# Kernel optimization log

Hardware: AMD Instinct MI355X
Metric: run time of the kernel (lower is better)

Reference implementation:

```python
import jax, jax.numpy as jnp
import numpy as np

T, B, IN, H, OUT = 345, 128, 13, 128, 9

# snnTorch ATan surrogate spike: forward = heaviside(x), backward = 1/(1+(pi*x)^2) (alpha=2)
@jax.custom_vjp
def spike_fn(x):
    return (x > 0).astype(x.dtype)

def _spike_fwd(x):
    return spike_fn(x), x

def _spike_bwd(x, g):
    return (g / (1.0 + (jnp.pi * x) ** 2),)

spike_fn.defvjp(_spike_fwd, _spike_bwd)


def setup_inputs() -> dict:
    key = jax.random.key(0)
    ks = jax.random.split(key, 5)
    x = jax.random.normal(ks[0], (B, IN, T), dtype=jnp.float32)
    # PyTorch Linear init: U(-1/sqrt(fan_in), 1/sqrt(fan_in))
    lim1 = 1.0 / np.sqrt(IN)
    lim2 = 1.0 / np.sqrt(H)
    W1 = jax.random.uniform(ks[1], (H, IN), minval=-lim1, maxval=lim1, dtype=jnp.float32)
    b1 = jax.random.uniform(ks[2], (H,), minval=-lim1, maxval=lim1, dtype=jnp.float32)
    W2 = jax.random.uniform(ks[3], (OUT, H), minval=-lim2, maxval=lim2, dtype=jnp.float32)
    b2 = jax.random.uniform(ks[4], (OUT,), minval=-lim2, maxval=lim2, dtype=jnp.float32)
    beta1 = jnp.float32(0.9)
    thr1 = jnp.float32(1.0)
    beta2 = jnp.float32(0.9)
    thr2 = jnp.float32(1.0)
    return {"x": x, "W1": W1, "b1": b1, "W2": W2, "b2": b2,
            "beta1": beta1, "thr1": thr1, "beta2": beta2, "thr2": thr2}


def reference(x, W1, b1, W2, b2, beta1, thr1, beta2, thr2):
    # Precompute fc1 for all steps: (T, B, H)
    cur1_all = jnp.einsum('bct,hc->tbh', x, W1) + b1
    bt1 = jnp.clip(beta1, 0.0, 1.0)
    bt2 = jnp.clip(beta2, 0.0, 1.0)

    def step(carry, cur1):
        mem1, mem2 = carry
        mem1 = bt1 * mem1 + cur1                 # leaky integrate
        spk1 = spike_fn(mem1 - thr1)             # fire
        mem1 = mem1 - spk1 * thr1                # subtract reset
        cur2 = spk1 @ W2.T + b2                  # (B, OUT)
        mem2 = bt2 * mem2 + cur2
        spk2 = spike_fn(mem2 - thr2)
        mem2 = mem2 - spk2 * thr2
        return (mem1, mem2), (spk2, mem2)

    init = (jnp.zeros((B, H), x.dtype), jnp.zeros((B, OUT), x.dtype))
    _, (spk_rec, mem_rec) = jax.lax.scan(step, init, cur1_all)
    return spk_rec, mem_rec  # each (T, B, OUT)
```

## Files before the change

### kernel.cpp

```cpp
#include <hip/hip_runtime.h>

#define T_STEPS 345
#define B_SZ    128
#define IN_SZ   13
#define H_SZ    128
#define OUT_SZ  9
#define XPITCH  16
#define TPAD    384
#define NBO     (B_SZ * OUT_SZ)
#define NCHUNK  22
#define MASK_BYTES (B_SZ * T_STEPS * 2 * 8)

__global__ __launch_bounds__(128, 1)
void k1_spikes(const float* __restrict__ x, const float* __restrict__ W1,
               const float* __restrict__ b1, const float* __restrict__ beta1p,
               const float* __restrict__ thr1p,
               unsigned long long* __restrict__ masks)
{
    const int b   = blockIdx.x;
    const int tid = threadIdx.x;

    __shared__ float xst[(T_STEPS + 3) * XPITCH];

    const float* xb = x + (size_t)b * (IN_SZ * T_STEPS);
    for (int i = tid; i < IN_SZ * T_STEPS; i += 128) {
        const int c = i / T_STEPS;
        const int t = i - c * T_STEPS;
        xst[t * XPITCH + c] = xb[i];
    }

    const float bt1 = fminf(fmaxf(beta1p[0], 0.0f), 1.0f);
    const float th1 = thr1p[0];

    float w1r[IN_SZ];
#pragma unroll
    for (int c = 0; c < IN_SZ; ++c) w1r[c] = W1[tid * IN_SZ + c];
    const float b1r = b1[tid];

    float mem1 = 0.0f;
    unsigned long long* mp = masks + (size_t)b * (T_STEPS * 2) + (tid >> 6);
    const bool store_lane = (tid & 63) == 0;

    __syncthreads();

    const float4* xq = (const float4*)xst;
    float4 a0 = xq[0], a1 = xq[1], a2 = xq[2]; float a3 = xst[12];
    float4 c0 = xq[4], c1 = xq[5], c2 = xq[6]; float c3 = xst[XPITCH + 12];

    int t = 0;
    for (; t < T_STEPS - 1; t += 2) {
        const float xa[IN_SZ] = { a0.x,a0.y,a0.z,a0.w, a1.x,a1.y,a1.z,a1.w,
                                  a2.x,a2.y,a2.z,a2.w, a3 };
        const float xc[IN_SZ] = { c0.x,c0.y,c0.z,c0.w, c1.x,c1.y,c1.z,c1.w,
                                  c2.x,c2.y,c2.z,c2.w, c3 };
        a0 = xq[(t+2)*4+0]; a1 = xq[(t+2)*4+1]; a2 = xq[(t+2)*4+2]; a3 = xst[(t+2)*XPITCH+12];
        c0 = xq[(t+3)*4+0]; c1 = xq[(t+3)*4+1]; c2 = xq[(t+3)*4+2]; c3 = xst[(t+3)*XPITCH+12];

        float cura = b1r, curb = b1r;
#pragma unroll
        for (int c = 0; c < IN_SZ; ++c) {
            cura = fmaf(xa[c], w1r[c], cura);
            curb = fmaf(xc[c], w1r[c], curb);
        }

        mem1 = fmaf(bt1, mem1, cura);
        const bool pa = mem1 > th1;
        const unsigned long long ma = __ballot(pa);
        mem1 = fmaf(pa ? -1.0f : 0.0f, th1, mem1);
        if (store_lane) mp[0] = ma;

        mem1 = fmaf(bt1, mem1, curb);
        const bool pb = mem1 > th1;
        const unsigned long long mb = __ballot(pb);
        mem1 = fmaf(pb ? -1.0f : 0.0f, th1, mem1);
        if (store_lane) mp[2] = mb;

        mp += 4;
    }
    {
        const float xa[IN_SZ] = { a0.x,a0.y,a0.z,a0.w, a1.x,a1.y,a1.z,a1.w,
                                  a2.x,a2.y,a2.z,a2.w, a3 };
        float cura = b1r;
#pragma unroll
        for (int c = 0; c < IN_SZ; ++c) cura = fmaf(xa[c], w1r[c], cura);
        mem1 = fmaf(bt1, mem1, cura);
        const bool pa = mem1 > th1;
        const unsigned long long ma = __ballot(pa);
        if (store_lane) mp[0] = ma;
    }
}

__global__ __launch_bounds__(256, 1)
void k2_gemm(const unsigned long long* __restrict__ masks,
             const float* __restrict__ W2, const float* __restrict__ b2,
             float* __restrict__ cur2)
{
    const int gw   = blockIdx.x * 4 + (threadIdx.x >> 6);
    const int lane = threadIdx.x & 63;
    const int bo   = gw / 6;
    const int w    = gw - bo * 6;
    const int b    = bo / 9;
    const int o    = bo - b * 9;
    const int t    = w * 64 + lane;
    const int tc   = (t < T_STEPS) ? t : (T_STEPS - 1);

    const uint4 mm = *(const uint4*)((const char*)masks +
                                     ((size_t)b * T_STEPS + tc) * 16);

    const float* __restrict__ w2row = W2 + o * H_SZ;
    float acc = 0.0f;
#pragma unroll
    for (int h = 0; h < 32; ++h)
        acc = fmaf((float)((mm.x >> h) & 1u), w2row[h], acc);
#pragma unroll
    for (int h = 0; h < 32; ++h)
        acc = fmaf((float)((mm.y >> h) & 1u), w2row[32 + h], acc);
#pragma unroll
    for (int h = 0; h < 32; ++h)
        acc = fmaf((float)((mm.z >> h) & 1u), w2row[64 + h], acc);
#pragma unroll
    for (int h = 0; h < 32; ++h)
        acc = fmaf((float)((mm.w >> h) & 1u), w2row[96 + h], acc);

    cur2[(size_t)t * NBO + bo] = acc + b2[o];
}

__global__ __launch_bounds__(64, 1)
void k3_scan2(const float* __restrict__ cur2, const float* __restrict__ beta2p,
              const float* __restrict__ thr2p, float* __restrict__ out)
{
    const int lid = blockIdx.x * 64 + threadIdx.x;
    const float bt2 = fminf(fmaxf(beta2p[0], 0.0f), 1.0f);
    const float th2 = thr2p[0];

    const float* __restrict__ src = cur2 + lid;
    float* __restrict__ out_spk = out + lid;
    float* __restrict__ out_mem = out + (size_t)T_STEPS * NBO + lid;

    float mem2 = 0.0f;

    float A[16], Bb[16];
#pragma unroll
    for (int j = 0; j < 16; ++j) A[j]  = src[(size_t)j * NBO];
#pragma unroll
    for (int j = 0; j < 16; ++j) Bb[j] = src[(size_t)(16 + j) * NBO];

    float sE[16], mE[16], sO[16], mO[16];

    for (int c = 0; c < NCHUNK; c += 2) {
#pragma unroll
        for (int j = 0; j < 16; ++j) {
            mem2 = fmaf(bt2, mem2, A[j]);
            const float sp = (mem2 > th2) ? 1.0f : 0.0f;
            mem2 = fmaf(-sp, th2, mem2);
            sE[j] = sp; mE[j] = mem2;
        }
        const int cn = (c + 2 < NCHUNK) ? (c + 2) : c;
#pragma unroll
        for (int j = 0; j < 16; ++j) A[j] = src[(size_t)(cn * 16 + j) * NBO];
        {
            const size_t base = (size_t)c * 16 * NBO;
#pragma unroll
            for (int j = 0; j < 16; ++j) {
                out_spk[base + (size_t)j * NBO] = sE[j];
                out_mem[base + (size_t)j * NBO] = mE[j];
            }
        }

#pragma unroll
        for (int j = 0; j < 16; ++j) {
            mem2 = fmaf(bt2, mem2, Bb[j]);
            const float sp = (mem2 > th2) ? 1.0f : 0.0f;
            mem2 = fmaf(-sp, th2, mem2);
            sO[j] = sp; mO[j] = mem2;
        }
        const int cn2 = (c + 3 < NCHUNK) ? (c + 3) : c;
#pragma unroll
        for (int j = 0; j < 16; ++j) Bb[j] = src[(size_t)(cn2 * 16 + j) * NBO];
        if (c + 1 < NCHUNK - 1) {
            const size_t base = (size_t)(c + 1) * 16 * NBO;
#pragma unroll
            for (int j = 0; j < 16; ++j) {
                out_spk[base + (size_t)j * NBO] = sO[j];
                out_mem[base + (size_t)j * NBO] = mO[j];
            }
        } else {
            const size_t base = (size_t)(c + 1) * 16 * NBO;
#pragma unroll
            for (int j = 0; j < 9; ++j) {
                out_spk[base + (size_t)j * NBO] = sO[j];
                out_mem[base + (size_t)j * NBO] = mO[j];
            }
        }
    }
}

extern "C" void kernel_launch(void* const* d_in, const int* in_sizes, int n_in,
                              void* d_out, int out_size, void* d_ws, size_t ws_size,
                              hipStream_t stream) {
    const float* x     = (const float*)d_in[0];
    const float* W1    = (const float*)d_in[1];
    const float* b1    = (const float*)d_in[2];
    const float* W2    = (const float*)d_in[3];
    const float* b2    = (const float*)d_in[4];
    const float* beta1 = (const float*)d_in[5];
    const float* thr1  = (const float*)d_in[6];
    const float* beta2 = (const float*)d_in[7];
    const float* thr2  = (const float*)d_in[8];
    float* out = (float*)d_out;

    char* ws = (char*)d_ws;
    unsigned long long* masks = (unsigned long long*)ws;
    float* cur2 = (float*)(ws + MASK_BYTES);

    k1_spikes<<<dim3(B_SZ), dim3(128), 0, stream>>>(x, W1, b1, beta1, thr1, masks);
    k2_gemm  <<<dim3(1728), dim3(256), 0, stream>>>(masks, W2, b2, cur2);
    k3_scan2 <<<dim3(NBO / 64), dim3(64), 0, stream>>>(cur2, beta2, thr2, out);
}
```

Measured before the change: 128.6 us.

## Fuse spike, GEMM and output scan kernels into one per-batch block

Merges the three kernels into one kernel with one block per batch element. Layer-1 spike masks and layer-2 currents stay in shared memory instead of being written to and read back from global workspace. The GEMM is restructured so each thread computes all 9 outputs for one timestep. The layer-2 scan now runs on only 9 threads per block with strided global stores, which reduces parallelism and coalescing in that phase.

```diff
diff --git a/kernel.cpp b/kernel.cpp
--- a/kernel.cpp
+++ b/kernel.cpp
@@ -6,190 +6,197 @@
 #define H_SZ    128
 #define OUT_SZ  9
 #define XPITCH  16
-#define TPAD    384
 #define NBO     (B_SZ * OUT_SZ)
 #define NCHUNK  22
-#define MASK_BYTES (B_SZ * T_STEPS * 2 * 8)
-
-__global__ __launch_bounds__(128, 1)
-void k1_spikes(const float* __restrict__ x, const float* __restrict__ W1,
-               const float* __restrict__ b1, const float* __restrict__ beta1p,
-               const float* __restrict__ thr1p,
-               unsigned long long* __restrict__ masks)
+#define TPADL   352
+
+__global__ __launch_bounds__(384, 1)
+void snn_fused(const float* __restrict__ x, const float* __restrict__ W1,
+               const float* __restrict__ b1, const float* __restrict__ W2,
+               const float* __restrict__ b2, const float* __restrict__ beta1p,
+               const float* __restrict__ thr1p, const float* __restrict__ beta2p,
+               const float* __restrict__ thr2p, float* __restrict__ out)
 {
     const int b   = blockIdx.x;
     const int tid = threadIdx.x;
 
     __shared__ float xst[(T_STEPS + 3) * XPITCH];
+    __shared__ __align__(16) unsigned long long msk[T_STEPS][2];
+    __shared__ float c2[TPADL * OUT_SZ];
 
     const float* xb = x + (size_t)b * (IN_SZ * T_STEPS);
-    for (int i = tid; i < IN_SZ * T_STEPS; i += 128) {
+    for (int i = tid; i < IN_SZ * T_STEPS; i += 384) {
         const int c = i / T_STEPS;
         const int t = i - c * T_STEPS;
         xst[t * XPITCH + c] = xb[i];
     }
-
-    const float bt1 = fminf(fmaxf(beta1p[0], 0.0f), 1.0f);
-    const float th1 = thr1p[0];
-
-    float w1r[IN_SZ];
-#pragma unroll
-    for (int c = 0; c < IN_SZ; ++c) w1r[c] = W1[tid * IN_SZ + c];
-    const float b1r = b1[tid];
-
-    float mem1 = 0.0f;
-    unsigned long long* mp = masks + (size_t)b * (T_STEPS * 2) + (tid >> 6);
-    const bool store_lane = (tid & 63) == 0;
-
     __syncthreads();
 
-    const float4* xq = (const float4*)xst;
-    float4 a0 = xq[0], a1 = xq[1], a2 = xq[2]; float a3 = xst[12];
-    float4 c0 = xq[4], c1 = xq[5], c2 = xq[6]; float c3 = xst[XPITCH + 12];
-
-    int t = 0;
-    for (; t < T_STEPS - 1; t += 2) {
-        const float xa[IN_SZ] = { a0.x,a0.y,a0.z,a0.w, a1.x,a1.y,a1.z,a1.w,
-                                  a2.x,a2.y,a2.z,a2.w, a3 };
-        const float xc[IN_SZ] = { c0.x,c0.y,c0.z,c0.w, c1.x,c1.y,c1.z,c1.w,
-                                  c2.x,c2.y,c2.z,c2.w, c3 };
-        a0 = xq[(t+2)*4+0]; a1 = xq[(t+2)*4+1]; a2 = xq[(t+2)*4+2]; a3 = xst[(t+2)*XPITCH+12];
-        c0 = xq[(t+3)*4+0]; c1 = xq[(t+3)*4+1]; c2 = xq[(t+3)*4+2]; c3 = xst[(t+3)*XPITCH+12];
-
-        float cura = b1r, curb = b1r;
-#pragma unroll
-        for (int c = 0; c < IN_SZ; ++c) {
-            cura = fmaf(xa[c], w1r[c], cura);
-            curb = fmaf(xc[c], w1r[c], curb);
-        }
-
-        mem1 = fmaf(bt1, mem1, cura);
-        const bool pa = mem1 > th1;
-        const unsigned long long ma = __ballot(pa);
-        mem1 = fmaf(pa ? -1.0f : 0.0f, th1, mem1);
-        if (store_lane) mp[0] = ma;
-
-        mem1 = fmaf(bt1, mem1, curb);
-        const bool pb = mem1 > th1;
-        const unsigned long long mb = __ballot(pb);
-        mem1 = fmaf(pb ? -1.0f : 0.0f, th1, mem1);
-        if (store_lane) mp[2] = mb;
-
-        mp += 4;
-    }
-    {
-        const float xa[IN_SZ] = { a0.x,a0.y,a0.z,a0.w, a1.x,a1.y,a1.z,a1.w,
-                                  a2.x,a2.y,a2.z,a2.w, a3 };
-        float cura = b1r;
-#pragma unroll
-        for (int c = 0; c < IN_SZ; ++c) cura = fmaf(xa[c], w1r[c], cura);
-        mem1 = fmaf(bt1, mem1, cura);
-        const bool pa = mem1 > th1;
-        const unsigned long long ma = __ballot(pa);
-        if (store_lane) mp[0] = ma;
-    }
-}
-
-__global__ __launch_bounds__(256, 1)
-void k2_gemm(const unsigned long long* __restrict__ masks,
-             const float* __restrict__ W2, const float* __restrict__ b2,
-             float* __restrict__ cur2)
-{
-    const int gw   = blockIdx.x * 4 + (threadIdx.x >> 6);
-    const int lane = threadIdx.x & 63;
-    const int bo   = gw / 6;
-    const int w    = gw - bo * 6;
-    const int b    = bo / 9;
-    const int o    = bo - b * 9;
-    const int t    = w * 64 + lane;
-    const int tc   = (t < T_STEPS) ? t : (T_STEPS - 1);
-
-    const uint4 mm = *(const uint4*)((const char*)masks +
-                                     ((size_t)b * T_STEPS + tc) * 16);
-
-    const float* __restrict__ w2row = W2 + o * H_SZ;
-    float acc = 0.0f;
-#pragma unroll
-    for (int h = 0; h < 32; ++h)
-        acc = fmaf((float)((mm.x >> h) & 1u), w2row[h], acc);
-#pragma unroll
-    for (int h = 0; h < 32; ++h)
-        acc = fmaf((float)((mm.y >> h) & 1u), w2row[32 + h], acc);
-#pragma unroll
-    for (int h = 0; h < 32; ++h)
-        acc = fmaf((float)((mm.z >> h) & 1u), w2row[64 + h], acc);
-#pragma unroll
-    for (int h = 0; h < 32; ++h)
-        acc = fmaf((float)((mm.w >> h) & 1u), w2row[96 + h], acc);
-
-    cur2[(size_t)t * NBO + bo] = acc + b2[o];
-}
-
-__global__ __launch_bounds__(64, 1)
-void k3_scan2(const float* __restrict__ cur2, const float* __restrict__ beta2p,
-              const float* __restrict__ thr2p, float* __restrict__ out)
-{
-    const int lid = blockIdx.x * 64 + threadIdx.x;
-    const float bt2 = fminf(fmaxf(beta2p[0], 0.0f), 1.0f);
-    const float th2 = thr2p[0];
-
-    const float* __restrict__ src = cur2 + lid;
-    float* __restrict__ out_spk = out + lid;
-    float* __restrict__ out_mem = out + (size_t)T_STEPS * NBO + lid;
-
-    float mem2 = 0.0f;
-
-    float A[16], Bb[16];
-#pragma unroll
-    for (int j = 0; j < 16; ++j) A[j]  = src[(size_t)j * NBO];
-#pragma unroll
-    for (int j = 0; j < 16; ++j) Bb[j] = src[(size_t)(16 + j) * NBO];
-
-    float sE[16], mE[16], sO[16], mO[16];
-
-    for (int c = 0; c < NCHUNK; c += 2) {
-#pragma unroll
-        for (int j = 0; j < 16; ++j) {
-            mem2 = fmaf(bt2, mem2, A[j]);
-            const float sp = (mem2 > th2) ? 1.0f : 0.0f;
-            mem2 = fmaf(-sp, th2, mem2);
-            sE[j] = sp; mE[j] = mem2;
-        }
-        const int cn = (c + 2 < NCHUNK) ? (c + 2) : c;
-#pragma unroll
-        for (int j = 0; j < 16; ++j) A[j] = src[(size_t)(cn * 16 + j) * NBO];
+    if (tid < 128) {
+        const float bt1 = fminf(fmaxf(beta1p[0], 0.0f), 1.0f);
+        const float th1 = thr1p[0];
+
+        float w1r[IN_SZ];
+#pragma unroll
+        for (int c = 0; c < IN_SZ; ++c) w1r[c] = W1[tid * IN_SZ + c];
+        const float b1r = b1[tid];
+
+        float mem1 = 0.0f;
+        const int half = tid >> 6;
+        const bool store_lane = (tid & 63) == 0;
+
+        const float4* xq = (const float4*)xst;
+        float4 a0 = xq[0], a1 = xq[1], a2 = xq[2]; float a3 = xst[12];
+        float4 c0 = xq[4], c1 = xq[5], c2r = xq[6]; float c3 = xst[XPITCH + 12];
+
+        int t = 0;
+        for (; t < T_STEPS - 1; t += 2) {
+            const float xa[IN_SZ] = { a0.x,a0.y,a0.z,a0.w, a1.x,a1.y,a1.z,a1.w,
+                                      a2.x,a2.y,a2.z,a2.w, a3 };
+            const float xc[IN_SZ] = { c0.x,c0.y,c0.z,c0.w, c1.x,c1.y,c1.z,c1.w,
+                                      c2r.x,c2r.y,c2r.z,c2r.w, c3 };
+            a0 = xq[(t+2)*4+0]; a1 = xq[(t+2)*4+1]; a2  = xq[(t+2)*4+2]; a3 = xst[(t+2)*XPITCH+12];
+            c0 = xq[(t+3)*4+0]; c1 = xq[(t+3)*4+1]; c2r = xq[(t+3)*4+2]; c3 = xst[(t+3)*XPITCH+12];
+
+            float cura = b1r, curb = b1r;
+#pragma unroll
+            for (int c = 0; c < IN_SZ; ++c) {
+                cura = fmaf(xa[c], w1r[c], cura);
+                curb = fmaf(xc[c], w1r[c], curb);
+            }
+
+            mem1 = fmaf(bt1, mem1, cura);
+            const bool pa = mem1 > th1;
+            const unsigned long long ma = __ballot(pa);
+            mem1 = fmaf(pa ? -1.0f : 0.0f, th1, mem1);
+            if (store_lane) msk[t][half] = ma;
+
+            mem1 = fmaf(bt1, mem1, curb);
+            const bool pb = mem1 > th1;
+            const unsigned long long mb = __ballot(pb);
+            mem1 = fmaf(pb ? -1.0f : 0.0f, th1, mem1);
+            if (store_lane) msk[t + 1][half] = mb;
+        }
         {
-            const size_t base = (size_t)c * 16 * NBO;
+            const float xa[IN_SZ] = { a0.x,a0.y,a0.z,a0.w, a1.x,a1.y,a1.z,a1.w,
+                                      a2.x,a2.y,a2.z,a2.w, a3 };
+            float cura = b1r;
+#pragma unroll
+            for (int c = 0; c < IN_SZ; ++c) cura = fmaf(xa[c], w1r[c], cura);
+            mem1 = fmaf(bt1, mem1, cura);
+            const bool pa = mem1 > th1;
+            const unsigned long long ma = __ballot(pa);
+            if (store_lane) msk[t][half] = ma;
+        }
+    }
+    __syncthreads();
+
+    if (tid < TPADL) {
+        const int t  = tid;
+        const int tc = (t < T_STEPS) ? t : (T_STEPS - 1);
+        const uint4 mm = *(const uint4*)&msk[tc][0];
+
+        float acc[OUT_SZ];
+#pragma unroll
+        for (int o = 0; o < OUT_SZ; ++o) acc[o] = 0.0f;
+
+#pragma unroll
+        for (int h = 0; h < 32; ++h) {
+            const float bit = (float)((mm.x >> h) & 1u);
+#pragma unroll
+            for (int o = 0; o < OUT_SZ; ++o)
+                acc[o] = fmaf(bit, W2[o * H_SZ + h], acc[o]);
+        }
+#pragma unroll
+        for (int h = 0; h < 32; ++h) {
+            const float bit = (float)((mm.y >> h) & 1u);
+#pragma unroll
+            for (int o = 0; o < OUT_SZ; ++o)
+                acc[o] = fmaf(bit, W2[o * H_SZ + 32 + h], acc[o]);
+        }
+#pragma unroll
+        for (int h = 0; h < 32; ++h) {
+            const float bit = (float)((mm.z >> h) & 1u);
+#pragma unroll
+            for (int o = 0; o < OUT_SZ; ++o)
+                acc[o] = fmaf(bit, W2[o * H_SZ + 64 + h], acc[o]);
+        }
+#pragma unroll
+        for (int h = 0; h < 32; ++h) {
+            const float bit = (float)((mm.w >> h) & 1u);
+#pragma unroll
+            for (int o = 0; o < OUT_SZ; ++o)
+                acc[o] = fmaf(bit, W2[o * H_SZ + 96 + h], acc[o]);
+        }
+
+#pragma unroll
+        for (int o = 0; o < OUT_SZ; ++o)
+            c2[t * OUT_SZ + o] = acc[o] + b2[o];
+    }
+    __syncthreads();
+
+    if (tid < OUT_SZ) {
+        const int o = tid;
+        const float bt2 = fminf(fmaxf(beta2p[0], 0.0f), 1.0f);
+        const float th2 = thr2p[0];
+
+        float* __restrict__ out_spk = out + (size_t)b * OUT_SZ + o;
+        float* __restrict__ out_mem = out + (size_t)T_STEPS * NBO + (size_t)b * OUT_SZ + o;
+
+        float mem2 = 0.0f;
+
+        float A[16], Bb[16];
+#pragma unroll
+        for (int j = 0; j < 16; ++j) A[j]  = c2[j * OUT_SZ + o];
+#pragma unroll
+        for (int j = 0; j < 16; ++j) Bb[j] = c2[(16 + j) * OUT_SZ + o];
+
+        float sE[16], mE[16], sO[16], mO[16];
+
+        for (int c = 0; c < NCHUNK; c += 2) {
 #pragma unroll
             for (int j = 0; j < 16; ++j) {
-                out_spk[base + (size_t)j * NBO] = sE[j];
-                out_mem[base + (size_t)j * NBO] = mE[j];
-            }
-        }
-
-#pragma unroll
-        for (int j = 0; j < 16; ++j) {
-            mem2 = fmaf(bt2, mem2, Bb[j]);
-            const float sp = (mem2 > th2) ? 1.0f : 0.0f;
-            mem2 = fmaf(-sp, th2, mem2);
-            sO[j] = sp; mO[j] = mem2;
-        }
-        const int cn2 = (c + 3 < NCHUNK) ? (c + 3) : c;
-#pragma unroll
-        for (int j = 0; j < 16; ++j) Bb[j] = src[(size_t)(cn2 * 16 + j) * NBO];
-        if (c + 1 < NCHUNK - 1) {
-            const size_t base = (size_t)(c + 1) * 16 * NBO;
+                mem2 = fmaf(bt2, mem2, A[j]);
+                const float sp = (mem2 > th2) ? 1.0f : 0.0f;
+                mem2 = fmaf(-sp, th2, mem2);
+                sE[j] = sp; mE[j] = mem2;
+            }
+            const int cn = (c + 2 < NCHUNK) ? (c + 2) : c;
+#pragma unroll
+            for (int j = 0; j < 16; ++j) A[j] = c2[(cn * 16 + j) * OUT_SZ + o];
+            {
+                const size_t base = (size_t)c * 16 * NBO;
+#pragma unroll
+                for (int j = 0; j < 16; ++j) {
+                    out_spk[base + (size_t)j * NBO] = sE[j];
+                    out_mem[base + (size_t)j * NBO] = mE[j];
+                }
+            }
+
 #pragma unroll
             for (int j = 0; j < 16; ++j) {
-                out_spk[base + (size_t)j * NBO] = sO[j];
-                out_mem[base + (size_t)j * NBO] = mO[j];
-            }
-        } else {
-            const size_t base = (size_t)(c + 1) * 16 * NBO;
-#pragma unroll
-            for (int j = 0; j < 9; ++j) {
-                out_spk[base + (size_t)j * NBO] = sO[j];
-                out_mem[base + (size_t)j * NBO] = mO[j];
+                mem2 = fmaf(bt2, mem2, Bb[j]);
+                const float sp = (mem2 > th2) ? 1.0f : 0.0f;
+                mem2 = fmaf(-sp, th2, mem2);
+                sO[j] = sp; mO[j] = mem2;
+            }
+            const int cn2 = (c + 3 < NCHUNK) ? (c + 3) : c;
+#pragma unroll
+            for (int j = 0; j < 16; ++j) Bb[j] = c2[(cn2 * 16 + j) * OUT_SZ + o];
+            if (c + 1 < NCHUNK - 1) {
+                const size_t base = (size_t)(c + 1) * 16 * NBO;
+#pragma unroll
+                for (int j = 0; j < 16; ++j) {
+                    out_spk[base + (size_t)j * NBO] = sO[j];
+                    out_mem[base + (size_t)j * NBO] = mO[j];
+                }
+            } else {
+                const size_t base = (size_t)(c + 1) * 16 * NBO;
+#pragma unroll
+                for (int j = 0; j < 9; ++j) {
+                    out_spk[base + (size_t)j * NBO] = sO[j];
+                    out_mem[base + (size_t)j * NBO] = mO[j];
+                }
             }
         }
     }
@@ -209,11 +216,6 @@
     const float* thr2  = (const float*)d_in[8];
     float* out = (float*)d_out;
 
-    char* ws = (char*)d_ws;
-    unsigned long long* masks = (unsigned long long*)ws;
-    float* cur2 = (float*)(ws + MASK_BYTES);
-
-    k1_spikes<<<dim3(B_SZ), dim3(128), 0, stream>>>(x, W1, b1, beta1, thr1, masks);
-    k2_gemm  <<<dim3(1728), dim3(256), 0, stream>>>(masks, W2, b2, cur2);
-    k3_scan2 <<<dim3(NBO / 64), dim3(64), 0, stream>>>(cur2, beta2, thr2, out);
+    snn_fused<<<dim3(B_SZ), dim3(384), 0, stream>>>(
+        x, W1, b1, W2, b2, beta1, thr1, beta2, thr2, out);
 }
```

New measurement: 131.9 us. +2.6%, slower.
